# Performance work log

Hardware: AMD Instinct MI355X
Metric: run time of the kernel (lower is better)

## Reference

```python
import jax, jax.numpy as jnp
import numpy as np

N_NODES = 100000   # number of nodes
N_EDGES = 20000    # number of hyperedges
N_INC = 800000     # incidence (node, hyperedge) pairs
TEXT_DIM = 384     # all-MiniLM-L6-v2 sentence embedding dim
HID = 128          # hidden_dim in _init_model


def setup_inputs() -> dict:
    key = jax.random.key(0)
    ks = jax.random.split(key, 16)
    s = 1.0 / np.sqrt(HID)
    inp = {
        "text_emb": jax.random.normal(ks[0], (N_NODES, TEXT_DIM), jnp.float32),
        "W_proj": jax.random.normal(ks[1], (TEXT_DIM, HID), jnp.float32) / np.sqrt(TEXT_DIM),
        "b_proj": jnp.zeros((HID,), jnp.float32),
        # weight generator 0 (Linear-ReLU-Dropout(eval)-Linear)
        "W1a": jax.random.normal(ks[2], (HID, HID), jnp.float32) * s,
        "b1a": jnp.zeros((HID,), jnp.float32),
        "W2a": jax.random.normal(ks[3], (HID, HID), jnp.float32) * s,
        "b2a": jnp.zeros((HID,), jnp.float32),
        # weight generator 1
        "W1b": jax.random.normal(ks[4], (HID, HID), jnp.float32) * s,
        "b1b": jnp.zeros((HID,), jnp.float32),
        "W2b": jax.random.normal(ks[5], (HID, HID), jnp.float32) * s,
        "b2b": jnp.zeros((HID,), jnp.float32),
        "node_idx": jax.random.randint(ks[6], (N_INC,), 0, N_NODES),
        "edge_idx": jax.random.randint(ks[7], (N_INC,), 0, N_EDGES),
    }
    return inp


def _segment_mean(vals, idx, num_segments):
    # vals: [E_inc, D]; idx: [E_inc] -> [num_segments, D]
    ssum = jax.ops.segment_sum(vals, idx, num_segments=num_segments)
    cnt = jax.ops.segment_sum(jnp.ones((idx.shape[0], 1), vals.dtype), idx,
                              num_segments=num_segments)
    return ssum / jnp.maximum(cnt, 1.0)


def reference(text_emb, W_proj, b_proj,
              W1a, b1a, W2a, b2a,
              W1b, b1b, W2b, b2b,
              node_idx, edge_idx):
    # text projection to hidden space: [N, 128]
    h = text_emb @ W_proj + b_proj
    gens = ((W1a, b1a, W2a, b2a), (W1b, b1b, W2b, b2b))
    for (W1, b1, W2, b2) in gens:  # 2 hypergraph layers (fixed by code)
        # hypernetwork: generate per-layer dynamic modulation from pooled context
        g = jnp.mean(h, axis=0)                               # [128]
        scale = jnp.maximum(g @ W1 + b1, 0.0) @ W2 + b2       # [128]
        # gather node -> hyperedge, aggregate (mean) per hyperedge
        e_feat = _segment_mean(h[node_idx], edge_idx, N_EDGES)   # [E, 128]
        # gather hyperedge -> node, aggregate (mean) per node (scatter)
        m = _segment_mean(e_feat[edge_idx], node_idx, N_NODES)   # [N, 128]
        h = jax.nn.relu(m * scale)
    return h
```

## Files before the change

### kernel.cpp

```cpp
#include <hip/hip_runtime.h>

#define N_NODES 100000
#define N_EDGES 20000
#define N_INC   800000
#define TDIM    384
#define HID     128
#define NOFF    800000
#define NKEYS   120000

#define PROJ_BLOCKS 1563
#define CNT_BLOCKS  512
#define FILL_BLOCKS 3125
#define EAGG_BLOCKS 5000
#define NAGG_BLOCKS 2500

typedef __attribute__((ext_vector_type(8))) short short8;
typedef __attribute__((ext_vector_type(4))) float floatx4;

static __device__ __forceinline__ unsigned short f32_bf16_rne(float f) {
  unsigned int u = __float_as_uint(f);
  unsigned int r = u + 0x7FFFu + ((u >> 16) & 1u);
  return (unsigned short)(r >> 16);
}

static __device__ __forceinline__ unsigned xcd_id() {
  unsigned x;
  asm volatile("s_getreg_b32 %0, hwreg(HW_REG_XCC_ID)" : "=s"(x));
  return x & 7u;
}

__global__ __launch_bounds__(64) void wprep_kernel(
    const float* __restrict__ W, unsigned short* __restrict__ Bh,
    unsigned short* __restrict__ Bl)
{
  int b = blockIdx.x;
  int lane = threadIdx.x;
  int kk = b >> 3, nt = b & 7;
  int col = lane & 15, quad = lane >> 4;
  size_t o = ((size_t)b * 64 + lane) * 8;
#pragma unroll
  for (int j = 0; j < 8; ++j) {
    int k = kk * 32 + quad * 8 + j;
    float w = W[(size_t)k * HID + nt * 16 + col];
    unsigned short h = f32_bf16_rne(w);
    float hf = __uint_as_float((unsigned int)h << 16);
    Bh[o + j] = h;
    Bl[o + j] = f32_bf16_rne(w - hf);
  }
}

__global__ __launch_bounds__(256) void proj_count_kernel(
    const float* __restrict__ A, const unsigned short* __restrict__ Bh,
    const unsigned short* __restrict__ Bl, const float* __restrict__ bias,
    unsigned short* __restrict__ Hb, float* __restrict__ gsum0,
    const int* __restrict__ node_idx, const int* __restrict__ edge_idx,
    int* __restrict__ ecp8, int* __restrict__ ncp8,
    int* __restrict__ rank_e, int* __restrict__ rank_n)
{
  __shared__ unsigned short BhS[512 * 8];
  __shared__ unsigned short BlS[512 * 8];
  __shared__ float red[4][HID];
  const int tid = threadIdx.x;

  if (blockIdx.x >= PROJ_BLOCKS) {
    unsigned x = xcd_id();
    int* my_e = ecp8 + (size_t)x * N_EDGES;
    int* my_n = ncp8 + (size_t)x * N_NODES;
    unsigned xtag = x << 28;
    int start = (blockIdx.x - PROJ_BLOCKS) * 256 + tid;
    for (int i = start; i < N_INC; i += CNT_BLOCKS * 256) {
      int ed = edge_idx[i];
      int nd = node_idx[i];
      int le = __hip_atomic_fetch_add(&my_e[ed], 1, __ATOMIC_RELAXED,
                                      __HIP_MEMORY_SCOPE_WORKGROUP);
      int ln = __hip_atomic_fetch_add(&my_n[nd], 1, __ATOMIC_RELAXED,
                                      __HIP_MEMORY_SCOPE_WORKGROUP);
      rank_e[i] = (int)(xtag | (unsigned)le);
      rank_n[i] = (int)(xtag | (unsigned)ln);
    }
    return;
  }

  const int wave = tid >> 6;
  const int lane = tid & 63;
  const int col = lane & 15;
  const int quad = lane >> 4;
  const int m0 = blockIdx.x * 64 + wave * 16;

  floatx4 acc[8];
#pragma unroll
  for (int nt = 0; nt < 8; ++nt) acc[nt] = (floatx4){0.f, 0.f, 0.f, 0.f};

  int r = m0 + col;
  if (r >= N_NODES) r = N_NODES - 1;
  const float* arow = A + (size_t)r * TDIM + quad * 8;

  float ra[8];
  *(float4*)(&ra[0]) = *(const float4*)(arow);
  *(float4*)(&ra[4]) = *(const float4*)(arow + 4);

  for (int kk = 0; kk < 12; ++kk) {
    short8 sh0 = *(const short8*)(Bh + ((size_t)kk * 512 + tid) * 8);
    short8 sh1 = *(const short8*)(Bh + ((size_t)kk * 512 + tid + 256) * 8);
    short8 sl0 = *(const short8*)(Bl + ((size_t)kk * 512 + tid) * 8);
    short8 sl1 = *(const short8*)(Bl + ((size_t)kk * 512 + tid + 256) * 8);
    __syncthreads();
    *(short8*)(BhS + (size_t)tid * 8) = sh0;
    *(short8*)(BhS + ((size_t)tid + 256) * 8) = sh1;
    *(short8*)(BlS + (size_t)tid * 8) = sl0;
    *(short8*)(BlS + ((size_t)tid + 256) * 8) = sl1;

    float rn[8];
    if (kk < 11) {
      *(float4*)(&rn[0]) = *(const float4*)(arow + (kk + 1) * 32);
      *(float4*)(&rn[4]) = *(const float4*)(arow + (kk + 1) * 32 + 4);
    }

    short8 ah, al;
#pragma unroll
    for (int j = 0; j < 8; ++j) {
      float f = ra[j];
      unsigned short h = f32_bf16_rne(f);
      float hf = __uint_as_float((unsigned int)h << 16);
      ah[j] = (short)h;
      al[j] = (short)f32_bf16_rne(f - hf);
    }
    __syncthreads();

#pragma unroll
    for (int nt = 0; nt < 8; ++nt) {
      short8 bh = *(const short8*)(BhS + ((size_t)nt * 64 + lane) * 8);
      short8 bl = *(const short8*)(BlS + ((size_t)nt * 64 + lane) * 8);
      acc[nt] = __builtin_amdgcn_mfma_f32_16x16x32_bf16(ah, bh, acc[nt], 0, 0, 0);
      acc[nt] = __builtin_amdgcn_mfma_f32_16x16x32_bf16(al, bh, acc[nt], 0, 0, 0);
      acc[nt] = __builtin_amdgcn_mfma_f32_16x16x32_bf16(ah, bl, acc[nt], 0, 0, 0);
    }
#pragma unroll
    for (int j = 0; j < 8; ++j) ra[j] = rn[j];
  }

#pragma unroll
  for (int nt = 0; nt < 8; ++nt) {
    float bv = bias[nt * 16 + col];
    float p = 0.f;
#pragma unroll
    for (int rr = 0; rr < 4; ++rr) {
      int row = m0 + quad * 4 + rr;
      float v = acc[nt][rr] + bv;
      if (row < N_NODES) {
        Hb[(size_t)row * HID + nt * 16 + col] = f32_bf16_rne(v);
        p += v;
      }
    }
    p += __shfl_xor(p, 16, 64);
    p += __shfl_xor(p, 32, 64);
    if (quad == 0) red[wave][nt * 16 + col] = p;
  }
  __syncthreads();
  if (tid < HID) {
    float a = red[0][tid] + red[1][tid] + red[2][tid] + red[3][tid];
    atomicAdd(&gsum0[(blockIdx.x & 7) * HID + tid], a);
  }
}

__global__ __launch_bounds__(256) void merge_shards_kernel(
    int* __restrict__ ecp8, int* __restrict__ ncp8, int* __restrict__ cnt)
{
  int k = blockIdx.x * 256 + threadIdx.x;
  if (k >= NKEYS) return;
  int* arr;
  int stride, key;
  if (k < N_EDGES) { arr = ecp8; stride = N_EDGES; key = k; }
  else             { arr = ncp8; stride = N_NODES; key = k - N_EDGES; }
  int s = 0;
#pragma unroll
  for (int x = 0; x < 8; ++x) {
    int v = arr[(size_t)x * stride + key];
    arr[(size_t)x * stride + key] = s;
    s += v;
  }
  cnt[k] = s;
}

__global__ __launch_bounds__(1024) void scan_block(const int* __restrict__ cnt,
                                                   int* __restrict__ ptr,
                                                   int* __restrict__ partials, int n)
{
  __shared__ int s[1024];
  int tid = threadIdx.x;
  int i = blockIdx.x * 1024 + tid;
  int v = (i < n) ? cnt[i] : 0;
  s[tid] = v;
  __syncthreads();
  for (int off = 1; off < 1024; off <<= 1) {
    int add = (tid >= off) ? s[tid - off] : 0;
    __syncthreads();
    s[tid] += add;
    __syncthreads();
  }
  if (i < n) ptr[i] = s[tid] - v;
  if (tid == 1023) partials[blockIdx.x] = s[1023];
}

__global__ __launch_bounds__(1024) void scan_partials(int* __restrict__ partials, int nb,
                                                      int* __restrict__ ptr, int n)
{
  __shared__ int s[1024];
  int tid = threadIdx.x;
  int v = (tid < nb) ? partials[tid] : 0;
  s[tid] = v;
  __syncthreads();
  for (int off = 1; off < 1024; off <<= 1) {
    int add = (tid >= off) ? s[tid - off] : 0;
    __syncthreads();
    s[tid] += add;
    __syncthreads();
  }
  if (tid < nb) partials[tid] = s[tid] - v;
  if (tid == 0) ptr[n] = s[1023];
}

__global__ void scan_add(int* __restrict__ ptr, const int* __restrict__ partials, int n)
{
  int i = blockIdx.x * 1024 + threadIdx.x;
  if (i >= n) return;
  ptr[i] += partials[blockIdx.x];
}

__global__ __launch_bounds__(256) void fill_kernel(
    const int* __restrict__ node_idx, const int* __restrict__ edge_idx,
    const int* __restrict__ rank_e, const int* __restrict__ rank_n,
    const int* __restrict__ eptr, const int* __restrict__ nptr,
    const int* __restrict__ ecp8, const int* __restrict__ ncp8,
    int* __restrict__ ecols, int* __restrict__ ncols)
{
  int i = blockIdx.x * 256 + threadIdx.x;
  int ed = edge_idx[i];
  int nd = node_idx[i];
  unsigned re = (unsigned)rank_e[i];
  unsigned rn = (unsigned)rank_n[i];
  int xe = re >> 28, le = (int)(re & 0x0FFFFFFFu);
  int xn = rn >> 28, ln = (int)(rn & 0x0FFFFFFFu);
  int p = eptr[ed] + ecp8[(size_t)xe * N_EDGES + ed] + le;
  int q = nptr[nd] - NOFF + ncp8[(size_t)xn * N_NODES + nd] + ln;
  __builtin_nontemporal_store(nd, &ecols[p]);
  __builtin_nontemporal_store(ed, &ncols[q]);
}

__global__ __launch_bounds__(256) void edge_agg_scale_kernel(
    const unsigned short* __restrict__ Hb, const int* __restrict__ eptr,
    const int* __restrict__ ecols, unsigned short* __restrict__ Eb,
    const float* __restrict__ gsum,
    const float* __restrict__ W1, const float* __restrict__ b1,
    const float* __restrict__ W2, const float* __restrict__ b2,
    float* __restrict__ scale)
{
  if (blockIdx.x >= EAGG_BLOCKS) {
    __shared__ float g[HID], t[HID];
    int c = threadIdx.x;
    if (c < HID) {
      float s = 0.f;
#pragma unroll
      for (int k = 0; k < 8; ++k) s += gsum[k * HID + c];
      g[c] = s * (1.0f / (float)N_NODES);
    }
    __syncthreads();
    if (c < HID) {
      float acc = b1[c];
#pragma unroll 8
      for (int k = 0; k < HID; ++k) acc += g[k] * W1[(size_t)k * HID + c];
      t[c] = fmaxf(acc, 0.f);
    }
    __syncthreads();
    if (c < HID) {
      float acc2 = b2[c];
#pragma unroll 8
      for (int k = 0; k < HID; ++k) acc2 += t[k] * W2[(size_t)k * HID + c];
      scale[c] = acc2;
    }
    return;
  }
  int gw = blockIdx.x * 4 + (threadIdx.x >> 6);
  int lane = threadIdx.x & 63;
  int p0 = eptr[gw], p1 = eptr[gw + 1];
  float ax0 = 0.f, ay0 = 0.f, ax1 = 0.f, ay1 = 0.f;
  float ax2 = 0.f, ay2 = 0.f, ax3 = 0.f, ay3 = 0.f;
  for (int base = p0; base < p1; base += 64) {
    int cnt = min(64, p1 - base);
    int idx = (base + lane < p1) ? ecols[base + lane] : 0;
    int j = 0;
    for (; j + 3 < cnt; j += 4) {
      int n0 = __shfl(idx, j, 64);
      int n1 = __shfl(idx, j + 1, 64);
      int n2 = __shfl(idx, j + 2, 64);
      int n3 = __shfl(idx, j + 3, 64);
      unsigned v0 = *(const unsigned*)(Hb + (size_t)n0 * HID + lane * 2);
      unsigned v1 = *(const unsigned*)(Hb + (size_t)n1 * HID + lane * 2);
      unsigned v2 = *(const unsigned*)(Hb + (size_t)n2 * HID + lane * 2);
      unsigned v3 = *(const unsigned*)(Hb + (size_t)n3 * HID + lane * 2);
      ax0 += __uint_as_float(v0 << 16); ay0 += __uint_as_float(v0 & 0xffff0000u);
      ax1 += __uint_as_float(v1 << 16); ay1 += __uint_as_float(v1 & 0xffff0000u);
      ax2 += __uint_as_float(v2 << 16); ay2 += __uint_as_float(v2 & 0xffff0000u);
      ax3 += __uint_as_float(v3 << 16); ay3 += __uint_as_float(v3 & 0xffff0000u);
    }
    for (; j < cnt; ++j) {
      int n0 = __shfl(idx, j, 64);
      unsigned v0 = *(const unsigned*)(Hb + (size_t)n0 * HID + lane * 2);
      ax0 += __uint_as_float(v0 << 16); ay0 += __uint_as_float(v0 & 0xffff0000u);
    }
  }
  float inv = 1.f / (float)max(p1 - p0, 1);
  float sx = ((ax0 + ax1) + (ax2 + ax3)) * inv;
  float sy = ((ay0 + ay1) + (ay2 + ay3)) * inv;
  unsigned pk = ((unsigned)f32_bf16_rne(sy) << 16) | f32_bf16_rne(sx);
  *(unsigned*)(Eb + (size_t)gw * HID + lane * 2) = pk;
}

__global__ __launch_bounds__(256) void node_agg_kernel(
    const unsigned short* __restrict__ Eb, const int* __restrict__ nptr,
    const int* __restrict__ ncols, const float* __restrict__ scale,
    unsigned short* __restrict__ Hb, float* __restrict__ H,
    float* __restrict__ gsum, int do_aux)
{
  __shared__ float red[4][HID];
  int wave = threadIdx.x >> 6, lane = threadIdx.x & 63;
  float2 sc = *(const float2*)(scale + lane * 2);
  float csx = 0.f, csy = 0.f;
  for (int gw = blockIdx.x * 4 + wave; gw < N_NODES; gw += NAGG_BLOCKS * 4) {
    int p0 = nptr[gw] - NOFF, p1 = nptr[gw + 1] - NOFF;
    float ax0 = 0.f, ay0 = 0.f, ax1 = 0.f, ay1 = 0.f;
    float ax2 = 0.f, ay2 = 0.f, ax3 = 0.f, ay3 = 0.f;
    for (int base = p0; base < p1; base += 64) {
      int cnt = min(64, p1 - base);
      int idx = (base + lane < p1) ? ncols[base + lane] : 0;
      int j = 0;
      for (; j + 3 < cnt; j += 4) {
        int e0 = __shfl(idx, j, 64);
        int e1 = __shfl(idx, j + 1, 64);
        int e2 = __shfl(idx, j + 2, 64);
        int e3 = __shfl(idx, j + 3, 64);
        unsigned v0 = *(const unsigned*)(Eb + (size_t)e0 * HID + lane * 2);
        unsigned v1 = *(const unsigned*)(Eb + (size_t)e1 * HID + lane * 2);
        unsigned v2 = *(const unsigned*)(Eb + (size_t)e2 * HID + lane * 2);
        unsigned v3 = *(const unsigned*)(Eb + (size_t)e3 * HID + lane * 2);
        ax0 += __uint_as_float(v0 << 16); ay0 += __uint_as_float(v0 & 0xffff0000u);
        ax1 += __uint_as_float(v1 << 16); ay1 += __uint_as_float(v1 & 0xffff0000u);
        ax2 += __uint_as_float(v2 << 16); ay2 += __uint_as_float(v2 & 0xffff0000u);
        ax3 += __uint_as_float(v3 << 16); ay3 += __uint_as_float(v3 & 0xffff0000u);
      }
      for (; j < cnt; ++j) {
        int e0 = __shfl(idx, j, 64);
        unsigned v0 = *(const unsigned*)(Eb + (size_t)e0 * HID + lane * 2);
        ax0 += __uint_as_float(v0 << 16); ay0 += __uint_as_float(v0 & 0xffff0000u);
      }
    }
    float inv = 1.f / (float)max(p1 - p0, 1);
    float ox = fmaxf(((ax0 + ax1) + (ax2 + ax3)) * inv * sc.x, 0.f);
    float oy = fmaxf(((ay0 + ay1) + (ay2 + ay3)) * inv * sc.y, 0.f);
    if (do_aux) {
      unsigned pk = ((unsigned)f32_bf16_rne(oy) << 16) | f32_bf16_rne(ox);
      *(unsigned*)(Hb + (size_t)gw * HID + lane * 2) = pk;
      csx += ox; csy += oy;
    } else {
      *(float2*)(H + (size_t)gw * HID + lane * 2) = make_float2(ox, oy);
    }
  }
  if (do_aux) {
    red[wave][lane * 2] = csx;
    red[wave][lane * 2 + 1] = csy;
    __syncthreads();
    if (threadIdx.x < HID) {
      int c = threadIdx.x;
      float a = red[0][c] + red[1][c] + red[2][c] + red[3][c];
      atomicAdd(&gsum[(blockIdx.x & 7) * HID + c], a);
    }
  }
}

extern "C" void kernel_launch(void* const* d_in, const int* in_sizes, int n_in,
                              void* d_out, int out_size, void* d_ws, size_t ws_size,
                              hipStream_t stream)
{
  const float* text = (const float*)d_in[0];
  const float* Wp   = (const float*)d_in[1];
  const float* bp   = (const float*)d_in[2];
  const float* W1a  = (const float*)d_in[3];
  const float* b1a  = (const float*)d_in[4];
  const float* W2a  = (const float*)d_in[5];
  const float* b2a  = (const float*)d_in[6];
  const float* W1b  = (const float*)d_in[7];
  const float* b1b  = (const float*)d_in[8];
  const float* W2b  = (const float*)d_in[9];
  const float* b2b  = (const float*)d_in[10];
  const int* node_idx = (const int*)d_in[11];
  const int* edge_idx = (const int*)d_in[12];
  float* H = (float*)d_out;

  char* ws = (char*)d_ws;
  int*   ecp8  = (int*)(ws + 0);
  int*   ncp8  = (int*)(ws + 640000);
  float* gsum0 = (float*)(ws + 3840000);
  float* gsum1 = (float*)(ws + 3844096);
  const size_t zero_bytes = 3848192;
  int*   cnt   = (int*)(ws + 3848192);
  int*   cptr  = (int*)(ws + 4328192);
  int*   eptr  = cptr;
  int*   nptr  = cptr + N_EDGES;
  int*   ecols = (int*)(ws + 4808208);
  int*   ncols = (int*)(ws + 8008208);
  float* scale0 = (float*)(ws + 11208208);
  float* scale1 = (float*)(ws + 11208720);
  int*   partials = (int*)(ws + 11209232);
  unsigned short* Eb = (unsigned short*)(ws + 11213328);
  unsigned short* Hb = (unsigned short*)(ws + 16333328);
  unsigned short* Bh = (unsigned short*)(ws + 4808208);
  unsigned short* Bl = (unsigned short*)(ws + 4906512);
  int*   rank_e = (int*)d_out;
  int*   rank_n = rank_e + N_INC;

  hipMemsetAsync(ws, 0, zero_bytes, stream);

  wprep_kernel<<<96, 64, 0, stream>>>(Wp, Bh, Bl);
  proj_count_kernel<<<PROJ_BLOCKS + CNT_BLOCKS, 256, 0, stream>>>(
      text, Bh, Bl, bp, Hb, gsum0, node_idx, edge_idx, ecp8, ncp8, rank_e, rank_n);

  merge_shards_kernel<<<(NKEYS + 255) / 256, 256, 0, stream>>>(ecp8, ncp8, cnt);
  scan_block<<<118, 1024, 0, stream>>>(cnt, cptr, partials, NKEYS);
  scan_partials<<<1, 1024, 0, stream>>>(partials, 118, cptr, NKEYS);
  scan_add<<<118, 1024, 0, stream>>>(cptr, partials, NKEYS);

  fill_kernel<<<FILL_BLOCKS, 256, 0, stream>>>(
      node_idx, edge_idx, rank_e, rank_n, eptr, nptr, ecp8, ncp8, ecols, ncols);

  edge_agg_scale_kernel<<<EAGG_BLOCKS + 1, 256, 0, stream>>>(
      Hb, eptr, ecols, Eb, gsum0, W1a, b1a, W2a, b2a, scale0);
  node_agg_kernel<<<NAGG_BLOCKS, 256, 0, stream>>>(
      Eb, nptr, ncols, scale0, Hb, H, gsum1, 1);

  edge_agg_scale_kernel<<<EAGG_BLOCKS + 1, 256, 0, stream>>>(
      Hb, eptr, ecols, Eb, gsum1, W1b, b1b, W2b, b2b, scale1);
  node_agg_kernel<<<NAGG_BLOCKS, 256, 0, stream>>>(
      Eb, nptr, ncols, scale1, Hb, H, gsum1, 0);
}
```

Baseline: 561.7 us.

## Double-buffer weight tiles in LDS and stage projection output for vectorized stores

The projection GEMM now double-buffers the Bh/Bl weight tiles in shared memory and prefetches the next tile's global loads one iteration ahead. This drops one of the two barriers per k-step and overlaps global loads with the MFMA work. The epilogue writes bf16 results into a shared-memory tile first, then stores them to Hb with coalesced 16-byte writes instead of scattered 2-byte stores. Shared memory use grows to 32KB per block, which may lower occupancy, and more registers are held live for the prefetch.

```diff
diff --git a/kernel.cpp b/kernel.cpp
--- a/kernel.cpp
+++ b/kernel.cpp
@@ -57,8 +57,7 @@
     int* __restrict__ ecp8, int* __restrict__ ncp8,
     int* __restrict__ rank_e, int* __restrict__ rank_n)
 {
-  __shared__ unsigned short BhS[512 * 8];
-  __shared__ unsigned short BlS[512 * 8];
+  __shared__ __align__(16) unsigned short SMEM[16384];
   __shared__ float red[4][HID];
   const int tid = threadIdx.x;
 
@@ -99,19 +98,26 @@
   *(float4*)(&ra[0]) = *(const float4*)(arow);
   *(float4*)(&ra[4]) = *(const float4*)(arow + 4);
 
+  short8 sh0 = *(const short8*)(Bh + (size_t)tid * 8);
+  short8 sh1 = *(const short8*)(Bh + ((size_t)tid + 256) * 8);
+  short8 sl0 = *(const short8*)(Bl + (size_t)tid * 8);
+  short8 sl1 = *(const short8*)(Bl + ((size_t)tid + 256) * 8);
+
   for (int kk = 0; kk < 12; ++kk) {
-    short8 sh0 = *(const short8*)(Bh + ((size_t)kk * 512 + tid) * 8);
-    short8 sh1 = *(const short8*)(Bh + ((size_t)kk * 512 + tid + 256) * 8);
-    short8 sl0 = *(const short8*)(Bl + ((size_t)kk * 512 + tid) * 8);
-    short8 sl1 = *(const short8*)(Bl + ((size_t)kk * 512 + tid + 256) * 8);
-    __syncthreads();
+    unsigned short* BhS = SMEM + (kk & 1) * 4096;
+    unsigned short* BlS = SMEM + 8192 + (kk & 1) * 4096;
     *(short8*)(BhS + (size_t)tid * 8) = sh0;
     *(short8*)(BhS + ((size_t)tid + 256) * 8) = sh1;
     *(short8*)(BlS + (size_t)tid * 8) = sl0;
     *(short8*)(BlS + ((size_t)tid + 256) * 8) = sl1;
 
+    short8 nh0, nh1, nl0, nl1;
     float rn[8];
     if (kk < 11) {
+      nh0 = *(const short8*)(Bh + ((size_t)(kk + 1) * 512 + tid) * 8);
+      nh1 = *(const short8*)(Bh + ((size_t)(kk + 1) * 512 + tid + 256) * 8);
+      nl0 = *(const short8*)(Bl + ((size_t)(kk + 1) * 512 + tid) * 8);
+      nl1 = *(const short8*)(Bl + ((size_t)(kk + 1) * 512 + tid + 256) * 8);
       *(float4*)(&rn[0]) = *(const float4*)(arow + (kk + 1) * 32);
       *(float4*)(&rn[4]) = *(const float4*)(arow + (kk + 1) * 32 + 4);
     }
@@ -135,28 +141,43 @@
       acc[nt] = __builtin_amdgcn_mfma_f32_16x16x32_bf16(al, bh, acc[nt], 0, 0, 0);
       acc[nt] = __builtin_amdgcn_mfma_f32_16x16x32_bf16(ah, bl, acc[nt], 0, 0, 0);
     }
-#pragma unroll
-    for (int j = 0; j < 8; ++j) ra[j] = rn[j];
-  }
-
+    if (kk < 11) {
+      sh0 = nh0; sh1 = nh1; sl0 = nl0; sl1 = nl1;
+#pragma unroll
+      for (int j = 0; j < 8; ++j) ra[j] = rn[j];
+    }
+  }
+
+  __syncthreads();
+  unsigned short* HbT = SMEM;
 #pragma unroll
   for (int nt = 0; nt < 8; ++nt) {
     float bv = bias[nt * 16 + col];
     float p = 0.f;
 #pragma unroll
     for (int rr = 0; rr < 4; ++rr) {
-      int row = m0 + quad * 4 + rr;
+      int rloc = wave * 16 + quad * 4 + rr;
       float v = acc[nt][rr] + bv;
-      if (row < N_NODES) {
-        Hb[(size_t)row * HID + nt * 16 + col] = f32_bf16_rne(v);
-        p += v;
-      }
+      HbT[rloc * HID + nt * 16 + col] = f32_bf16_rne(v);
+      if (blockIdx.x * 64 + rloc < N_NODES) p += v;
     }
     p += __shfl_xor(p, 16, 64);
     p += __shfl_xor(p, 32, 64);
     if (quad == 0) red[wave][nt * 16 + col] = p;
   }
   __syncthreads();
+
+  const int rbase = blockIdx.x * 64;
+#pragma unroll
+  for (int pass = 0; pass < 4; ++pass) {
+    int idx = pass * 256 + tid;
+    int rloc = idx >> 4;
+    int coff = (idx & 15) * 8;
+    int grow = rbase + rloc;
+    if (grow < N_NODES)
+      *(short8*)(Hb + (size_t)grow * HID + coff) = *(const short8*)(HbT + rloc * HID + coff);
+  }
+
   if (tid < HID) {
     float a = red[0][tid] + red[1][tid] + red[2][tid] + red[3][tid];
     atomicAdd(&gsum0[(blockIdx.x & 7) * HID + tid], a);
```

After: 577.4 us. 1.03x slower.
